# Kernel tuning notes

Measured on AMD Instinct MI355X. Metric: run time of the kernel, lower is better.

## Reference

```python
import jax, jax.numpy as jnp
import numpy as np

LEAK = 0.01  # F.leaky_relu default negative_slope
TAU = 1.0    # sinkhorn_tau
ITERS = 5    # sinkhorn_iters


def leaky_relu(x):
    return jnp.where(x >= 0, x, LEAK * x)


def setup_inputs() -> dict:
    key = jax.random.key(0)
    B, N, F, E, H, L = 512, 200, 32, 128, 128, 2
    ks = jax.random.split(key, 8)
    def s(k, shape, fan_in):
        return jax.random.normal(k, shape, dtype=jnp.float32) * (1.0 / np.sqrt(fan_in)).astype(np.float32)
    return {
        "x": jax.random.normal(ks[0], (B, N, F), dtype=jnp.float32),
        "w_emb": s(ks[1], (E, F), F),
        "b_emb": jnp.zeros((E,), jnp.float32),
        "w_ih": s(ks[2], (L, 4 * H, E), H),   # stacked per-layer LSTM input weights
        "w_hh": s(ks[3], (L, 4 * H, H), H),   # stacked per-layer LSTM recurrent weights
        "b_ih": jnp.zeros((L, 4 * H), jnp.float32),
        "b_hh": jnp.zeros((L, 4 * H), jnp.float32),
        "w_fc1": s(ks[4], (E, H), H),
        "b_fc1": jnp.zeros((E,), jnp.float32),
        "w_fc2": s(ks[5], (N, E), E),
        "b_fc2": jnp.zeros((N,), jnp.float32),
        "do_round": 0,  # non-differentiable Hungarian rounding path disabled
    }


def _lstm_layer(xs, h0, c0, Wih, Whh, b):
    # xs: [N, B, E]  (seq-major, like torch.nn.LSTM); h0, c0: [B, H]
    def step(carry, x_t):
        h, c = carry
        g = x_t @ Wih.T + h @ Whh.T + b               # [B, 4H]
        i, f, gg, o = jnp.split(g, 4, axis=-1)        # torch gate order i,f,g,o
        c = jax.nn.sigmoid(f) * c + jax.nn.sigmoid(i) * jnp.tanh(gg)
        h = jax.nn.sigmoid(o) * jnp.tanh(c)
        return (h, c), h
    (hN, cN), hs = jax.lax.scan(step, (h0, c0), xs)
    return hs, hN, cN


def _sinkhorn(M, tau, n_iters):
    # exp(M / tau) followed by alternating row / column normalization
    x = jnp.exp(M / tau)
    for _ in range(n_iters):
        x = x / jnp.sum(x, axis=2, keepdims=True)  # row normalize
        x = x / jnp.sum(x, axis=1, keepdims=True)  # column normalize
    return x


def reference(x, w_emb, b_emb, w_ih, w_hh, b_ih, b_hh, w_fc1, b_fc1, w_fc2, b_fc2, do_round):
    # do_round=0: the Hungarian rounding branch (host round-trip) is skipped;
    # the module then returns just the Sinkhorn output psi.
    B = x.shape[0]
    H = w_hh.shape[-1]
    e = leaky_relu(x @ w_emb.T + b_emb)            # [B, N, E]
    xs = jnp.transpose(e, (1, 0, 2))               # [N, B, E]
    h = jnp.zeros((B, H), x.dtype)
    c = jnp.zeros((B, H), x.dtype)
    hs = xs
    # NB: original code feeds the SAME embedded x to every LSTM layer,
    # carrying only the (h, c) state between layers.
    for l in range(w_ih.shape[0]):
        hs, h, c = _lstm_layer(xs, h, c, w_ih[l], w_hh[l], b_ih[l] + b_hh[l])
    out = jnp.transpose(hs, (1, 0, 2))             # [B, N, H]
    out = leaky_relu(out @ w_fc1.T + b_fc1)        # [B, N, E]
    M = out @ w_fc2.T + b_fc2                      # [B, N, N]
    psi = _sinkhorn(M, TAU, ITERS)
    return psi
```

## Files before the change

kernel.cpp:

```cpp
#include <hip/hip_runtime.h>
#include <cstdint>
#include <cstddef>

#define LEAK 0.01f
#define L2E 1.4426950408889634f

typedef _Float16 f16;
typedef __attribute__((ext_vector_type(4))) _Float16 f16x4;
typedef __attribute__((ext_vector_type(8))) _Float16 f16x8;
typedef __attribute__((ext_vector_type(4))) float f32x4;
typedef __attribute__((ext_vector_type(2))) unsigned u32x2;

static __device__ __forceinline__ f16x8 pack8s(float4 a, float4 b, float s) {
  f16x8 r;
  r[0] = (f16)(a.x * s); r[1] = (f16)(a.y * s); r[2] = (f16)(a.z * s); r[3] = (f16)(a.w * s);
  r[4] = (f16)(b.x * s); r[5] = (f16)(b.y * s); r[6] = (f16)(b.z * s); r[7] = (f16)(b.w * s);
  return r;
}
static __device__ __forceinline__ f16x8 pack8(float4 a, float4 b) {
  return pack8s(a, b, 1.0f);
}
#define MFMA16(a, b, c) __builtin_amdgcn_mfma_f32_16x16x32_f16((a), (b), (c), 0, 0, 0)

static __device__ __forceinline__ void barrier_lds() {
  asm volatile("s_waitcnt lgkmcnt(0)\n\ts_barrier" ::: "memory");
}

static __device__ __forceinline__ float permswap_lo(float a, float b) {
  u32x2 r = __builtin_amdgcn_permlane32_swap(__float_as_uint(a),
                                             __float_as_uint(b), false, false);
  return __uint_as_float(r[0]);
}

__constant__ float SCG[4] = {L2E, L2E, 2.0f * L2E, L2E};

__global__ __launch_bounds__(256) void k_emb(
    const float* __restrict__ x, const float* __restrict__ wemb,
    const float* __restrict__ bemb, f16* __restrict__ e) {
  const int t = blockIdx.x, tid = threadIdx.x;
  __shared__ __align__(16) float wl[128 * 32];
  __shared__ float bl[128];
  for (int idx = tid; idx < 1024; idx += 256)
    ((float4*)wl)[idx] = ((const float4*)wemb)[idx];
  if (tid < 128) bl[tid] = bemb[tid];

  float xa[32], xb[32];
  const float* xpa = x + ((size_t)tid * 200 + t) * 32;
  const float* xpb = x + ((size_t)(tid + 256) * 200 + t) * 32;
#pragma unroll
  for (int k4 = 0; k4 < 8; ++k4) {
    float4 va = *(const float4*)(xpa + k4 * 4);
    float4 vb = *(const float4*)(xpb + k4 * 4);
    xa[k4 * 4 + 0] = va.x; xa[k4 * 4 + 1] = va.y; xa[k4 * 4 + 2] = va.z; xa[k4 * 4 + 3] = va.w;
    xb[k4 * 4 + 0] = vb.x; xb[k4 * 4 + 1] = vb.y; xb[k4 * 4 + 2] = vb.z; xb[k4 * 4 + 3] = vb.w;
  }
  __syncthreads();

  f16* ea = e + ((size_t)t * 512 + tid) * 128;
  f16* eb = e + ((size_t)t * 512 + tid + 256) * 128;
  for (int j8 = 0; j8 < 16; ++j8) {
    f16x8 oa, ob;
#pragma unroll
    for (int jj = 0; jj < 8; ++jj) {
      int j = j8 * 8 + jj;
      float aa = bl[j], ab = bl[j];
#pragma unroll
      for (int k4 = 0; k4 < 8; ++k4) {
        float4 wv = *(const float4*)&wl[j * 32 + k4 * 4];
        aa += xa[k4 * 4 + 0] * wv.x + xa[k4 * 4 + 1] * wv.y +
              xa[k4 * 4 + 2] * wv.z + xa[k4 * 4 + 3] * wv.w;
        ab += xb[k4 * 4 + 0] * wv.x + xb[k4 * 4 + 1] * wv.y +
              xb[k4 * 4 + 2] * wv.z + xb[k4 * 4 + 3] * wv.w;
      }
      oa[jj] = (f16)(aa >= 0.f ? aa : LEAK * aa);
      ob[jj] = (f16)(ab >= 0.f ? ab : LEAK * ab);
    }
    *(f16x8*)(ea + j8 * 8) = oa;
    *(f16x8*)(eb + j8 * 8) = ob;
  }
}

static __device__ __forceinline__ void xp_waves(
    const f16* __restrict__ e, const float* __restrict__ wih,
    const float* __restrict__ bih, const float* __restrict__ bhh,
    f16* __restrict__ xp, int t0, int wid, int ntasks, int stride, int lane) {
  const int q = lane >> 4, l16 = lane & 15;
  const int ct = wid & 7;

  f16x8 BW[4][4];
  float bias[4];
#pragma unroll
  for (int G = 0; G < 4; ++G) {
    int n = G * 128 + ct * 16 + l16;
    bias[G] = (bih[n] + bhh[n]) * SCG[G];
#pragma unroll
    for (int kc = 0; kc < 4; ++kc) {
      const float4* p = (const float4*)(wih + (size_t)n * 128 + kc * 32 + q * 8);
      BW[G][kc] = pack8s(p[0], p[1], SCG[G]);
    }
  }
  for (int task = wid; task < ntasks; task += stride) {
    int g2 = task >> 3;
    int tl = g2 >> 2, btg = g2 & 3;
#pragma unroll
    for (int p = 0; p < 8; ++p) {
      int bt = btg * 8 + p;
      const f16* A = e + ((size_t)(t0 + tl) * 512 + bt * 16 + l16) * 128 + q * 8;
      f16x8 af[4];
#pragma unroll
      for (int kc = 0; kc < 4; ++kc) af[kc] = *(const f16x8*)(A + kc * 32);
      f32x4 acc[4];
#pragma unroll
      for (int G = 0; G < 4; ++G)
        acc[G] = (f32x4){bias[G], bias[G], bias[G], bias[G]};
#pragma unroll
      for (int kc = 0; kc < 4; ++kc)
#pragma unroll
        for (int G = 0; G < 4; ++G)
          acc[G] = MFMA16(af[kc], BW[G][kc], acc[G]);
      f16x8 oA, oB;
#pragma unroll
      for (int r = 0; r < 4; ++r) {
        oA[r]     = (f16)acc[0][r];
        oA[4 + r] = (f16)acc[1][r];
        oB[r]     = (f16)acc[2][r];
        oB[4 + r] = (f16)acc[3][r];
      }
      f16* dst = xp + (size_t)tl * 262144 + bt * 8192 + ct * 1024 + lane * 16;
      *(f16x8*)dst = oA;
      *(f16x8*)(dst + 8) = oB;
    }
  }
}

__global__ __launch_bounds__(256, 2) void k_xp(
    const f16* __restrict__ e, const float* __restrict__ wih,
    const float* __restrict__ bih, const float* __restrict__ bhh,
    f16* __restrict__ xp, int t0) {
  const int nt = gridDim.x * 4;
  xp_waves(e, wih, bih, bhh, xp, t0,
           blockIdx.x * 4 + (threadIdx.x >> 6), nt, nt, threadIdx.x & 63);
}

static __device__ __forceinline__ void rec_body(
    const f16* __restrict__ xp, const float* __restrict__ whh,
    float* __restrict__ hws, float* __restrict__ cws,
    f16* __restrict__ hs, int layer, int t0, int CH, int bt) {
  const int tid = threadIdx.x;
  const int w = tid >> 6, lane = tid & 63, q = lane >> 4, l16 = lane & 15;
  const int row0 = (q & 1) * 4 + (q >> 1) * 2;
  __shared__ __align__(16) f16 hlds[2][8][136];

  f16x8 BH[4][4];
#pragma unroll
  for (int G = 0; G < 4; ++G) {
    int n = G * 128 + w * 16 + l16;
#pragma unroll
    for (int kc = 0; kc < 4; ++kc) {
      const float4* ph = (const float4*)(whh + (size_t)n * 128 + kc * 32 + q * 8);
      BH[G][kc] = pack8s(ph[0], ph[1], SCG[G]);
    }
  }

  float cst0, cst1;
  if (layer == 0 && t0 == 0) {
    cst0 = 0.f; cst1 = 0.f;
    for (int idx = tid; idx < 8 * 136; idx += 512)
      (&hlds[1][0][0])[idx] = (f16)0.f;
  } else {
    const float* cp = cws + ((size_t)(bt * 8 + w) * 64 + lane) * 2;
    cst0 = cp[0]; cst1 = cp[1];
    const float* hp = hws + ((size_t)(bt * 8 + w) * 64 + lane) * 2;
    hlds[1][row0 + 0][w * 16 + l16] = (f16)hp[0];
    hlds[1][row0 + 1][w * 16 + l16] = (f16)hp[1];
  }
  barrier_lds();

  const int qo = (bt & 1) * 2 + (q & 1);
  const f16* xpl = xp + (((size_t)(bt >> 1) * 8 + w) * 64 + qo * 16 + l16) * 16;
  f16x8 xa = *(const f16x8*)(xpl);
  f16x8 xb = *(const f16x8*)(xpl + 8);
  const int t1 = (CH > 1) ? 1 : 0;
  f16x8 n1a = *(const f16x8*)(xpl + (size_t)t1 * 262144);
  f16x8 n1b = *(const f16x8*)(xpl + (size_t)t1 * 262144 + 8);

  float hk0 = 0.f, hk1 = 0.f;
  for (int tl = 0; tl < CH; ++tl) {
    int tn2 = (tl + 2 < CH) ? tl + 2 : CH - 1;
    const f16* xpn = xpl + (size_t)tn2 * 262144;
    f16x8 n2a = *(const f16x8*)(xpn);
    f16x8 n2b = *(const f16x8*)(xpn + 8);

    const int rb = (tl + 1) & 1;
    f16x8 ah[4];
#pragma unroll
    for (int kc = 0; kc < 4; ++kc)
      ah[kc] = *(const f16x8*)&hlds[rb][l16 & 7][kc * 32 + q * 8];

    f32x4 acc[4];
#pragma unroll
    for (int r = 0; r < 4; ++r) {
      acc[0][r] = (float)xa[r];
      acc[1][r] = (float)xa[4 + r];
      acc[2][r] = (float)xb[r];
      acc[3][r] = (float)xb[4 + r];
    }
#pragma unroll
    for (int kc = 0; kc < 4; ++kc)
#pragma unroll
      for (int G = 0; G < 4; ++G)
        acc[G] = MFMA16(ah[kc], BH[G][kc], acc[G]);

    float e0[4], e1[4];
#pragma unroll
    for (int G = 0; G < 4; ++G) {
      e0[G] = permswap_lo(acc[G][0], acc[G][2]);
      e1[G] = permswap_lo(acc[G][1], acc[G][3]);
    }

    const int wb = tl & 1;
    f16 h16_0, h16_1;
#pragma unroll
    for (int j = 0; j < 2; ++j) {
      float gi = j ? e1[0] : e0[0];
      float gf = j ? e1[1] : e0[1];
      float gg = j ? e1[2] : e0[2];
      float go = j ? e1[3] : e0[3];
      float cprev = j ? cst1 : cst0;
      float ui = __builtin_amdgcn_exp2f(-gi);
      float uf = __builtin_amdgcn_exp2f(-gf);
      float ug = __builtin_amdgcn_exp2f(-fmaxf(gg, -88.f));
      float uo = __builtin_amdgcn_exp2f(-go);
      float sf = __builtin_amdgcn_rcpf(1.0f + uf);
      float p1 = (1.0f - ug) * __builtin_amdgcn_rcpf((1.0f + ui) * (1.0f + ug));
      float cc = sf * cprev + p1;
      if (j) cst1 = cc; else cst0 = cc;
      float ccl = fminf(fmaxf(cc, -30.f), 30.f) * (-2.0f * L2E);
      float ucc = __builtin_amdgcn_exp2f(ccl);
      float hv = (1.0f - ucc) * __builtin_amdgcn_rcpf((1.0f + uo) * (1.0f + ucc));
      if (j) { hk1 = hv; h16_1 = (f16)hv; } else { hk0 = hv; h16_0 = (f16)hv; }
      hlds[wb][row0 + j][w * 16 + l16] = j ? h16_1 : h16_0;
    }
    if (layer != 0) {
      f16* hp0 = hs + ((size_t)(bt * 8 + row0) * 200 + (t0 + tl)) * 128 + w * 16 + l16;
      hp0[0] = h16_0;
      hp0[25600] = h16_1;
    }
    barrier_lds();
    xa = n1a; xb = n1b; n1a = n2a; n1b = n2b;
  }

  float* hp = hws + ((size_t)(bt * 8 + w) * 64 + lane) * 2;
  hp[0] = hk0; hp[1] = hk1;
  float* cp = cws + ((size_t)(bt * 8 + w) * 64 + lane) * 2;
  cp[0] = cst0; cp[1] = cst1;
}

__global__ __launch_bounds__(512, 2) void k_rec(
    const f16* __restrict__ xp, const float* __restrict__ whh,
    float* __restrict__ hws, float* __restrict__ cws,
    f16* __restrict__ hs, int layer, int t0, int CH) {
  rec_body(xp, whh, hws, cws, hs, layer, t0, CH, blockIdx.x);
}

__global__ __launch_bounds__(512, 2) void k_recxp(
    const f16* __restrict__ xp_r, const float* __restrict__ whh,
    float* __restrict__ hws, float* __restrict__ cws,
    f16* __restrict__ hs, int layer, int t0_r,
    const f16* __restrict__ e, const float* __restrict__ wih_n,
    const float* __restrict__ bih_n, const float* __restrict__ bhh_n,
    f16* __restrict__ xp_w, int t0_x) {
  if (blockIdx.x < 64) {
    rec_body(xp_r, whh, hws, cws, hs, layer, t0_r, 100, blockIdx.x);
  } else {
    xp_waves(e, wih_n, bih_n, bhh_n, xp_w, t0_x,
             (blockIdx.x - 64) * 8 + (threadIdx.x >> 6), 3200, 1536,
             threadIdx.x & 63);
  }
}

__global__ __launch_bounds__(512, 4) void k_head(
    const f16* __restrict__ hs, const float* __restrict__ wfc1,
    const float* __restrict__ bfc1, const float* __restrict__ wfc2,
    const float* __restrict__ bfc2, float* __restrict__ psi) {
  extern __shared__ char smem[];
  f16* E = (f16*)smem;
  f16* o1 = (f16*)(smem + 27200);
  float* uu = (float*)(smem + 80000);
  float* vv = (float*)(smem + 80800);
  const int b = blockIdx.x, tid = threadIdx.x;
  const int w = tid >> 6, lane = tid & 63, q = lane >> 4, l16 = lane & 15;
  const f16* A = hs + (size_t)b * 200 * 128;

  f16x8 BF1[4];
  float bias1;
  {
    int n = w * 16 + l16;
    bias1 = bfc1[n];
#pragma unroll
    for (int kc = 0; kc < 4; ++kc) {
      const float4* p = (const float4*)(wfc1 + (size_t)n * 128 + kc * 32 + q * 8);
      BF1[kc] = pack8(p[0], p[1]);
    }
  }
  f16x8 BF2[2][4];
  float bias2[2] = {0.f, 0.f};
#pragma unroll
  for (int ci = 0; ci < 2; ++ci) {
    int ct = w + ci * 8;
    if (ct < 13) {
      int n = ct * 16 + l16; if (n > 199) n = 199;
      bias2[ci] = bfc2[n];
#pragma unroll
      for (int kc = 0; kc < 4; ++kc) {
        const float4* p = (const float4*)(wfc2 + (size_t)n * 128 + kc * 32 + q * 8);
        BF2[ci][kc] = pack8(p[0], p[1]);
      }
    }
  }

  for (int rt = 0; rt < 13; ++rt) {
    int m = rt * 16 + l16; if (m > 199) m = 199;
    f16x8 af[4];
#pragma unroll
    for (int kc = 0; kc < 4; ++kc)
      af[kc] = *(const f16x8*)(A + (size_t)m * 128 + kc * 32 + q * 8);
    f32x4 acc = (f32x4){bias1, bias1, bias1, bias1};
#pragma unroll
    for (int kc = 0; kc < 4; ++kc) acc = MFMA16(af[kc], BF1[kc], acc);
    int col = w * 16 + l16;
#pragma unroll
    for (int r = 0; r < 4; ++r) {
      int row = rt * 16 + q * 4 + r;
      float vvv = acc[r]; vvv = vvv >= 0.f ? vvv : LEAK * vvv;
      if (row < 200) o1[row * 136 + col] = (f16)vvv;
    }
  }
  __syncthreads();

  for (int rt = 0; rt < 13; ++rt) {
    int m = rt * 16 + l16; if (m > 199) m = 199;
    f16x8 af[4];
#pragma unroll
    for (int kc = 0; kc < 4; ++kc)
      af[kc] = *(const f16x8*)&o1[m * 136 + kc * 32 + q * 8];
    __syncthreads();
#pragma unroll
    for (int ci = 0; ci < 2; ++ci) {
      int ct = w + ci * 8;
      if (ct < 13) {
        f32x4 acc = (f32x4){bias2[ci], bias2[ci], bias2[ci], bias2[ci]};
#pragma unroll
        for (int kc = 0; kc < 4; ++kc) acc = MFMA16(af[kc], BF2[ci][kc], acc);
        int col = ct * 16 + l16;
#pragma unroll
        for (int r = 0; r < 4; ++r) {
          int row = rt * 16 + q * 4 + r;
          if (row < 200 && col < 200) E[row * 200 + col] = (f16)__expf(acc[r]);
        }
      }
    }
  }
  __syncthreads();
  if (tid < 200) vv[tid] = 1.0f;
  __syncthreads();

  for (int it = 0; it < 5; ++it) {
    if (tid < 400) {
      int r = tid >> 1, h = tid & 1;
      const f16* Er = E + r * 200 + h * 100;
      const float* vp = vv + h * 100;
      float s0 = 0.f, s1 = 0.f;
      for (int j = 0; j < 100; j += 4) {
        f16x4 e4 = *(const f16x4*)(Er + j);
        float4 v4 = *(const float4*)(vp + j);
        s0 += (float)e4[0] * v4.x + (float)e4[1] * v4.y;
        s1 += (float)e4[2] * v4.z + (float)e4[3] * v4.w;
      }
      float s = s0 + s1;
      s += __shfl_xor(s, 1);
      if (h == 0) uu[r] = __builtin_amdgcn_rcpf(s);
    }
    __syncthreads();
    if (tid < 400) {
      int c4 = tid >> 3, g = tid & 7;
      const f16* Ec = E + (size_t)(g * 25) * 200 + c4 * 4;
      float a0 = 0.f, a1 = 0.f, a2 = 0.f, a3 = 0.f;
      for (int i = 0; i < 25; ++i) {
        f16x4 e4 = *(const f16x4*)(Ec + i * 200);
        float ui = uu[g * 25 + i];
        a0 += (float)e4[0] * ui;
        a1 += (float)e4[1] * ui;
        a2 += (float)e4[2] * ui;
        a3 += (float)e4[3] * ui;
      }
#pragma unroll
      for (int mk = 1; mk <= 4; mk <<= 1) {
        a0 += __shfl_xor(a0, mk);
        a1 += __shfl_xor(a1, mk);
        a2 += __shfl_xor(a2, mk);
        a3 += __shfl_xor(a3, mk);
      }
      if (g == 0) {
        float4 o;
        o.x = __builtin_amdgcn_rcpf(a0);
        o.y = __builtin_amdgcn_rcpf(a1);
        o.z = __builtin_amdgcn_rcpf(a2);
        o.w = __builtin_amdgcn_rcpf(a3);
        *(float4*)(vv + c4 * 4) = o;
      }
    }
    __syncthreads();
  }

  float* P = psi + (size_t)b * 40000;
  for (int idx4 = tid; idx4 < 10000; idx4 += 512) {
    unsigned i = ((unsigned)idx4 * 5243u) >> 18;
    unsigned jq = (unsigned)idx4 - i * 50u;
    f16x4 e4 = *(const f16x4*)(E + i * 200 + jq * 4);
    float4 v4 = *(const float4*)(vv + jq * 4);
    float ui = uu[i];
    float4 o;
    o.x = ui * (float)e4[0] * v4.x;
    o.y = ui * (float)e4[1] * v4.y;
    o.z = ui * (float)e4[2] * v4.z;
    o.w = ui * (float)e4[3] * v4.w;
    *(float4*)(P + i * 200 + jq * 4) = o;
  }
}

extern "C" void kernel_launch(void* const* d_in, const int* in_sizes, int n_in,
                              void* d_out, int out_size, void* d_ws, size_t ws_size,
                              hipStream_t stream) {
  const float* x    = (const float*)d_in[0];
  const float* wemb = (const float*)d_in[1];
  const float* bemb = (const float*)d_in[2];
  const float* wih  = (const float*)d_in[3];
  const float* whh  = (const float*)d_in[4];
  const float* bih  = (const float*)d_in[5];
  const float* bhh  = (const float*)d_in[6];
  const float* wfc1 = (const float*)d_in[7];
  const float* bfc1 = (const float*)d_in[8];
  const float* wfc2 = (const float*)d_in[9];
  const float* bfc2 = (const float*)d_in[10];
  float* psi = (float*)d_out;

  char* ws = (char*)d_ws;
  f16*   e   = (f16*)(ws);
  float* hws = (float*)(ws + 26214400);
  float* cws = (float*)(ws + 26476544);
  f16*   hs  = (f16*)(ws + 26738688);
  f16*   xpA = (f16*)(ws + 52953088);
  f16*   xpB = (f16*)(ws + 105381888);

  const size_t fixed = 52953088;
  const bool pipelined = (ws_size >= 157810688ull);

  (void)hipFuncSetAttribute((const void*)k_head,
                            hipFuncAttributeMaxDynamicSharedMemorySize, 81600);

  k_emb<<<200, 256, 0, stream>>>(x, wemb, bemb, e);

  const float* wih1 = wih + 65536;  const float* whh1 = whh + 65536;
  const float* bih1 = bih + 512;    const float* bhh1 = bhh + 512;

  if (pipelined) {
    k_xp<<<800, 256, 0, stream>>>(e, wih, bih, bhh, xpA, 0);
    k_recxp<<<256, 512, 0, stream>>>(xpA, whh, hws, cws, hs, 0, 0,
                                     e, wih, bih, bhh, xpB, 100);
    k_recxp<<<256, 512, 0, stream>>>(xpB, whh, hws, cws, hs, 0, 100,
                                     e, wih1, bih1, bhh1, xpA, 0);
    k_recxp<<<256, 512, 0, stream>>>(xpA, whh1, hws, cws, hs, 1, 0,
                                     e, wih1, bih1, bhh1, xpB, 100);
    k_rec<<<64, 512, 0, stream>>>(xpB, whh1, hws, cws, hs, 1, 100, 100);
  } else {
    const int cands[] = {100, 50, 40, 25, 20, 10, 8, 5, 4, 2, 1};
    int CH = 1;
    for (int ci = 0; ci < 11; ++ci) {
      if (fixed + (size_t)cands[ci] * 524288 <= ws_size) { CH = cands[ci]; break; }
    }
    for (int l = 0; l < 2; ++l) {
      const float* wih_l = wih + (size_t)l * 65536;
      const float* whh_l = whh + (size_t)l * 65536;
      const float* bih_l = bih + (size_t)l * 512;
      const float* bhh_l = bhh + (size_t)l * 512;
      for (int t0 = 0; t0 < 200; t0 += CH) {
        k_xp<<<CH * 8, 256, 0, stream>>>(e, wih_l, bih_l, bhh_l, xpA, t0);
        k_rec<<<64, 512, 0, stream>>>(xpA, whh_l, hws, cws, hs, l, t0, CH);
      }
    }
  }
  k_head<<<512, 512, 81600, stream>>>(hs, wfc1, bfc1, wfc2, bfc2, psi);
}
```

Before: 551.0 us.

## Fuse embedding into LSTM input projection and reschedule pipelined layer chunks

```diff
diff --git a/kernel.cpp b/kernel.cpp
--- a/kernel.cpp
+++ b/kernel.cpp
@@ -142,14 +142,124 @@
            blockIdx.x * 4 + (threadIdx.x >> 6), nt, nt, threadIdx.x & 63);
 }
 
+static __device__ __forceinline__ void xp_lds_layer(
+    const f16* e_lds, const float* __restrict__ wih,
+    const float* __restrict__ bih, const float* __restrict__ bhh,
+    f16* __restrict__ xp, int tl, int ct, int lane) {
+  const int q = lane >> 4, l16 = lane & 15;
+  f16x8 BW[4][4];
+  float bias[4];
+#pragma unroll
+  for (int G = 0; G < 4; ++G) {
+    int n = G * 128 + ct * 16 + l16;
+    bias[G] = (bih[n] + bhh[n]) * SCG[G];
+#pragma unroll
+    for (int kc = 0; kc < 4; ++kc) {
+      const float4* p = (const float4*)(wih + (size_t)n * 128 + kc * 32 + q * 8);
+      BW[G][kc] = pack8s(p[0], p[1], SCG[G]);
+    }
+  }
+  for (int bt = 0; bt < 32; ++bt) {
+    f16x8 af[4];
+#pragma unroll
+    for (int kc = 0; kc < 4; ++kc)
+      af[kc] = *(const f16x8*)&e_lds[(bt * 16 + l16) * 136 + kc * 32 + q * 8];
+    f32x4 acc[4];
+#pragma unroll
+    for (int G = 0; G < 4; ++G)
+      acc[G] = (f32x4){bias[G], bias[G], bias[G], bias[G]};
+#pragma unroll
+    for (int kc = 0; kc < 4; ++kc)
+#pragma unroll
+      for (int G = 0; G < 4; ++G)
+        acc[G] = MFMA16(af[kc], BW[G][kc], acc[G]);
+    f16x8 oA, oB;
+#pragma unroll
+    for (int r = 0; r < 4; ++r) {
+      oA[r]     = (f16)acc[0][r];
+      oA[4 + r] = (f16)acc[1][r];
+      oB[r]     = (f16)acc[2][r];
+      oB[4 + r] = (f16)acc[3][r];
+    }
+    f16* dst = xp + (size_t)tl * 262144 + bt * 8192 + ct * 1024 + lane * 16;
+    *(f16x8*)dst = oA;
+    *(f16x8*)(dst + 8) = oB;
+  }
+}
+
+static __device__ void embxp_block(
+    const float* __restrict__ x, const float* __restrict__ wemb,
+    const float* __restrict__ bemb,
+    const float* __restrict__ wih0, const float* __restrict__ bih0,
+    const float* __restrict__ bhh0, f16* __restrict__ xp0, int tl0,
+    const float* __restrict__ wih1, const float* __restrict__ bih1,
+    const float* __restrict__ bhh1, f16* __restrict__ xp1, int tl1,
+    int t, char* smem) {
+  f16* e_lds = (f16*)smem;
+  float* wl  = (float*)(smem + 139264);
+  float* bl  = (float*)(smem + 155648);
+  const int tid = threadIdx.x;
+  for (int idx = tid; idx < 1024; idx += 512)
+    ((float4*)wl)[idx] = ((const float4*)wemb)[idx];
+  if (tid < 128) bl[tid] = bemb[tid];
+
+  float xr[32];
+  const float* xptr = x + ((size_t)tid * 200 + t) * 32;
+#pragma unroll
+  for (int k4 = 0; k4 < 8; ++k4) {
+    float4 v = *(const float4*)(xptr + k4 * 4);
+    xr[k4 * 4 + 0] = v.x; xr[k4 * 4 + 1] = v.y;
+    xr[k4 * 4 + 2] = v.z; xr[k4 * 4 + 3] = v.w;
+  }
+  __syncthreads();
+
+  for (int j8 = 0; j8 < 16; ++j8) {
+    f16x8 o;
+#pragma unroll
+    for (int jj = 0; jj < 8; ++jj) {
+      int j = j8 * 8 + jj;
+      float a = bl[j];
+#pragma unroll
+      for (int k4 = 0; k4 < 8; ++k4) {
+        float4 wv = *(const float4*)&wl[j * 32 + k4 * 4];
+        a += xr[k4 * 4 + 0] * wv.x + xr[k4 * 4 + 1] * wv.y +
+             xr[k4 * 4 + 2] * wv.z + xr[k4 * 4 + 3] * wv.w;
+      }
+      o[jj] = (f16)(a >= 0.f ? a : LEAK * a);
+    }
+    *(f16x8*)&e_lds[tid * 136 + j8 * 8] = o;
+  }
+  __syncthreads();
+
+  const int w = tid >> 6, lane = tid & 63;
+  xp_lds_layer(e_lds, wih0, bih0, bhh0, xp0, tl0, w, lane);
+  if (xp1) xp_lds_layer(e_lds, wih1, bih1, bhh1, xp1, tl1, w, lane);
+}
+
+__global__ __launch_bounds__(512, 2) void k_embxp(
+    const float* __restrict__ x, const float* __restrict__ wemb,
+    const float* __restrict__ bemb,
+    const float* __restrict__ wih0, const float* __restrict__ bih0,
+    const float* __restrict__ bhh0,
+    const float* __restrict__ wih1, const float* __restrict__ bih1,
+    const float* __restrict__ bhh1,
+    f16* __restrict__ bufA, f16* __restrict__ bufB, f16* __restrict__ bufC) {
+  extern __shared__ char smem[];
+  const int t = blockIdx.x;
+  f16* xp0 = (t < 100) ? bufA : bufB;
+  int tl0 = (t < 100) ? t : t - 100;
+  f16* xp1 = (t < 100) ? bufC : nullptr;
+  embxp_block(x, wemb, bemb, wih0, bih0, bhh0, xp0, tl0,
+              wih1, bih1, bhh1, xp1, (t < 100) ? t : 0, t, smem);
+}
+
 static __device__ __forceinline__ void rec_body(
     const f16* __restrict__ xp, const float* __restrict__ whh,
     float* __restrict__ hws, float* __restrict__ cws,
-    f16* __restrict__ hs, int layer, int t0, int CH, int bt) {
+    f16* __restrict__ hs, int layer, int t0, int CH, f16* hlds, int bt) {
   const int tid = threadIdx.x;
   const int w = tid >> 6, lane = tid & 63, q = lane >> 4, l16 = lane & 15;
   const int row0 = (q & 1) * 4 + (q >> 1) * 2;
-  __shared__ __align__(16) f16 hlds[2][8][136];
 
   f16x8 BH[4][4];
 #pragma unroll
@@ -166,13 +276,13 @@
   if (layer == 0 && t0 == 0) {
     cst0 = 0.f; cst1 = 0.f;
     for (int idx = tid; idx < 8 * 136; idx += 512)
-      (&hlds[1][0][0])[idx] = (f16)0.f;
+      hlds[8 * 136 + idx] = (f16)0.f;
   } else {
     const float* cp = cws + ((size_t)(bt * 8 + w) * 64 + lane) * 2;
     cst0 = cp[0]; cst1 = cp[1];
     const float* hp = hws + ((size_t)(bt * 8 + w) * 64 + lane) * 2;
-    hlds[1][row0 + 0][w * 16 + l16] = (f16)hp[0];
-    hlds[1][row0 + 1][w * 16 + l16] = (f16)hp[1];
+    hlds[(8 + row0 + 0) * 136 + w * 16 + l16] = (f16)hp[0];
+    hlds[(8 + row0 + 1) * 136 + w * 16 + l16] = (f16)hp[1];
   }
   barrier_lds();
 
@@ -195,7 +305,7 @@
     f16x8 ah[4];
 #pragma unroll
     for (int kc = 0; kc < 4; ++kc)
-      ah[kc] = *(const f16x8*)&hlds[rb][l16 & 7][kc * 32 + q * 8];
+      ah[kc] = *(const f16x8*)&hlds[(rb * 8 + (l16 & 7)) * 136 + kc * 32 + q * 8];
 
     f32x4 acc[4];
 #pragma unroll
@@ -239,7 +349,7 @@
       float ucc = __builtin_amdgcn_exp2f(ccl);
       float hv = (1.0f - ucc) * __builtin_amdgcn_rcpf((1.0f + uo) * (1.0f + ucc));
       if (j) { hk1 = hv; h16_1 = (f16)hv; } else { hk0 = hv; h16_0 = (f16)hv; }
-      hlds[wb][row0 + j][w * 16 + l16] = j ? h16_1 : h16_0;
+      hlds[(wb * 8 + row0 + j) * 136 + w * 16 + l16] = j ? h16_1 : h16_0;
     }
     if (layer != 0) {
       f16* hp0 = hs + ((size_t)(bt * 8 + row0) * 200 + (t0 + tl)) * 128 + w * 16 + l16;
@@ -260,22 +370,24 @@
     const f16* __restrict__ xp, const float* __restrict__ whh,
     float* __restrict__ hws, float* __restrict__ cws,
     f16* __restrict__ hs, int layer, int t0, int CH) {
-  rec_body(xp, whh, hws, cws, hs, layer, t0, CH, blockIdx.x);
-}
-
-__global__ __launch_bounds__(512, 2) void k_recxp(
+  extern __shared__ char smem[];
+  rec_body(xp, whh, hws, cws, hs, layer, t0, CH, (f16*)smem, blockIdx.x);
+}
+
+__global__ __launch_bounds__(512, 2) void k_recxp2(
     const f16* __restrict__ xp_r, const float* __restrict__ whh,
-    float* __restrict__ hws, float* __restrict__ cws,
-    f16* __restrict__ hs, int layer, int t0_r,
-    const f16* __restrict__ e, const float* __restrict__ wih_n,
-    const float* __restrict__ bih_n, const float* __restrict__ bhh_n,
-    f16* __restrict__ xp_w, int t0_x) {
+    float* __restrict__ hws, float* __restrict__ cws, f16* __restrict__ hs,
+    const float* __restrict__ x, const float* __restrict__ wemb,
+    const float* __restrict__ bemb,
+    const float* __restrict__ wih1, const float* __restrict__ bih1,
+    const float* __restrict__ bhh1, f16* __restrict__ xp_w) {
+  extern __shared__ char smem[];
   if (blockIdx.x < 64) {
-    rec_body(xp_r, whh, hws, cws, hs, layer, t0_r, 100, blockIdx.x);
+    rec_body(xp_r, whh, hws, cws, hs, 0, 100, 100, (f16*)smem, blockIdx.x);
   } else {
-    xp_waves(e, wih_n, bih_n, bhh_n, xp_w, t0_x,
-             (blockIdx.x - 64) * 8 + (threadIdx.x >> 6), 3200, 1536,
-             threadIdx.x & 63);
+    int t = 100 + (blockIdx.x - 64);
+    embxp_block(x, wemb, bemb, wih1, bih1, bhh1, xp_w, t - 100,
+                nullptr, nullptr, nullptr, nullptr, 0, t, smem);
   }
 }
 
@@ -446,39 +558,51 @@
   float* psi = (float*)d_out;
 
   char* ws = (char*)d_ws;
-  f16*   e   = (f16*)(ws);
-  float* hws = (float*)(ws + 26214400);
-  float* cws = (float*)(ws + 26476544);
-  f16*   hs  = (f16*)(ws + 26738688);
-  f16*   xpA = (f16*)(ws + 52953088);
-  f16*   xpB = (f16*)(ws + 105381888);
-
-  const size_t fixed = 52953088;
-  const bool pipelined = (ws_size >= 157810688ull);
+  const float* wih1 = wih + 65536;  const float* whh1 = whh + 65536;
+  const float* bih1 = bih + 512;    const float* bhh1 = bhh + 512;
 
   (void)hipFuncSetAttribute((const void*)k_head,
                             hipFuncAttributeMaxDynamicSharedMemorySize, 81600);
 
-  k_emb<<<200, 256, 0, stream>>>(x, wemb, bemb, e);
-
-  const float* wih1 = wih + 65536;  const float* whh1 = whh + 65536;
-  const float* bih1 = bih + 512;    const float* bhh1 = bhh + 512;
+  const bool pipelined = (ws_size >= 157810688ull);
 
   if (pipelined) {
-    k_xp<<<800, 256, 0, stream>>>(e, wih, bih, bhh, xpA, 0);
-    k_recxp<<<256, 512, 0, stream>>>(xpA, whh, hws, cws, hs, 0, 0,
-                                     e, wih, bih, bhh, xpB, 100);
-    k_recxp<<<256, 512, 0, stream>>>(xpB, whh, hws, cws, hs, 0, 100,
-                                     e, wih1, bih1, bhh1, xpA, 0);
-    k_recxp<<<256, 512, 0, stream>>>(xpA, whh1, hws, cws, hs, 1, 0,
-                                     e, wih1, bih1, bhh1, xpB, 100);
-    k_rec<<<64, 512, 0, stream>>>(xpB, whh1, hws, cws, hs, 1, 100, 100);
+    f16* bufA = (f16*)(ws);
+    f16* bufB = (f16*)(ws + 52428800);
+    f16* bufC = (f16*)(ws + 104857600);
+    float* hws = (float*)(ws + 157286400);
+    float* cws = (float*)(ws + 157548544);
+    f16* hs = bufB;
+
+    (void)hipFuncSetAttribute((const void*)k_embxp,
+                              hipFuncAttributeMaxDynamicSharedMemorySize, 156160);
+    (void)hipFuncSetAttribute((const void*)k_recxp2,
+                              hipFuncAttributeMaxDynamicSharedMemorySize, 156160);
+
+    k_embxp<<<200, 512, 156160, stream>>>(x, wemb, bemb,
+                                          wih, bih, bhh, wih1, bih1, bhh1,
+                                          bufA, bufB, bufC);
+    k_rec<<<64, 512, 4608, stream>>>(bufA, whh, hws, cws, hs, 0, 0, 100);
+    k_recxp2<<<164, 512, 156160, stream>>>(bufB, whh, hws, cws, hs,
+                                           x, wemb, bemb,
+                                           wih1, bih1, bhh1, bufA);
+    k_rec<<<64, 512, 4608, stream>>>(bufC, whh1, hws, cws, hs, 1, 0, 100);
+    k_rec<<<64, 512, 4608, stream>>>(bufA, whh1, hws, cws, hs, 1, 100, 100);
+
+    k_head<<<512, 512, 81600, stream>>>(hs, wfc1, bfc1, wfc2, bfc2, psi);
   } else {
+    f16*   e   = (f16*)(ws);
+    float* hws = (float*)(ws + 26214400);
+    float* cws = (float*)(ws + 26476544);
+    f16*   hs  = (f16*)(ws + 26738688);
+    f16*   xpA = (f16*)(ws + 52953088);
+    const size_t fixed = 52953088;
     const int cands[] = {100, 50, 40, 25, 20, 10, 8, 5, 4, 2, 1};
     int CH = 1;
     for (int ci = 0; ci < 11; ++ci) {
       if (fixed + (size_t)cands[ci] * 524288 <= ws_size) { CH = cands[ci]; break; }
     }
+    k_emb<<<200, 256, 0, stream>>>(x, wemb, bemb, e);
     for (int l = 0; l < 2; ++l) {
       const float* wih_l = wih + (size_t)l * 65536;
       const float* whh_l = whh + (size_t)l * 65536;
@@ -486,9 +610,9 @@
       const float* bhh_l = bhh + (size_t)l * 512;
       for (int t0 = 0; t0 < 200; t0 += CH) {
         k_xp<<<CH * 8, 256, 0, stream>>>(e, wih_l, bih_l, bhh_l, xpA, t0);
-        k_rec<<<64, 512, 0, stream>>>(xpA, whh_l, hws, cws, hs, l, t0, CH);
-      }
-    }
-  }
-  k_head<<<512, 512, 81600, stream>>>(hs, wfc1, bfc1, wfc2, bfc2, psi);
-}
+        k_rec<<<64, 512, 4608, stream>>>(xpA, whh_l, hws, cws, hs, l, t0, CH);
+      }
+    }
+    k_head<<<512, 512, 81600, stream>>>(hs, wfc1, bfc1, wfc2, bfc2, psi);
+  }
+}
```

Result: slower. 562.9 us (+2.2%).
